# Kernel optimization log

Hardware: AMD Instinct MI355X
Metric: run time of the kernel (lower is better)

## Reference

```python
import jax, jax.numpy as jnp
import numpy as np

DISCOUNT = 0.99
HORIZON = 16


def setup_inputs() -> dict:
    key = jax.random.key(0)
    k1, k2, k3 = jax.random.split(key, 3)
    T, B = 1024, 4096
    rewards = jax.random.normal(k1, (T, B), dtype=jnp.float32)
    values = jax.random.normal(k2, (T, B), dtype=jnp.float32)
    masks = jax.random.uniform(k3, (T, B), dtype=jnp.float32)
    return {"rewards": rewards, "values": values, "masks": masks}


def _n_step_return(rewards, values, masks, gamma, horizon):
    # rewards/values/masks: [T, B]; time_axis == 0
    T = rewards.shape[0]
    rm = rewards * masks  # masked rewards
    # Pad end of time axis with zeros so every window has length `horizon`;
    # out-of-range rewards contribute 0, matching the truncated MC sum.
    pad = jnp.zeros((horizon - 1,) + rm.shape[1:], rm.dtype)
    rm_p = jnp.concatenate([rm, pad], axis=0)  # [T + horizon - 1, B]
    t = jnp.arange(T)
    idx = t[:, None] + jnp.arange(horizon)[None, :]  # [T, horizon]
    windows = rm_p[idx]  # [T, horizon, B]
    disc = jnp.asarray(gamma, rm.dtype) ** jnp.arange(horizon, dtype=rm.dtype)
    g = jnp.einsum('thb,h->tb', windows, disc)  # windowed discounted sums
    # Bootstrap: gamma^{effective_horizon} * V(s_{min(t+horizon-1, T-1)})
    eff_h = (jnp.minimum(t + horizon, T) - t).astype(rm.dtype)  # [T]
    v_idx = jnp.minimum(t + horizon - 1, T - 1)  # [T]
    g = g + (jnp.asarray(gamma, rm.dtype) ** eff_h)[:, None] * values[v_idx]
    return g


def reference(rewards, values, masks):
    return _n_step_return(rewards, values, masks, DISCOUNT, HORIZON)
```

## Files before the change

### kernel.cpp

```cpp
#include <hip/hip_runtime.h>


constexpr int   T_DIM  = 1024;
constexpr int   B_DIM  = 4096;
constexpr int   B4     = B_DIM / 4;
constexpr int   H      = 16;
constexpr int   CT     = 8;
constexpr int   HALO   = H - 1;
constexpr int   ROWS   = CT + HALO;
constexpr float GAMMA  = 0.99f;

constexpr float gpow_c(int n) {
    float g = 1.0f;
    for (int i = 0; i < n; ++i) g *= GAMMA;
    return g;
}
constexpr float G16 = gpow_c(16);

__device__ __forceinline__ float4 f4_mul(float4 a, float4 b) {
    return make_float4(a.x * b.x, a.y * b.y, a.z * b.z, a.w * b.w);
}
__device__ __forceinline__ float4 f4_fma(float s, float4 a, float4 b) {
    return make_float4(fmaf(s, a.x, b.x), fmaf(s, a.y, b.y),
                       fmaf(s, a.z, b.z), fmaf(s, a.w, b.w));
}

__global__ __launch_bounds__(256, 2)
void NStepReturn_88691074662796_kernel(const float4* __restrict__ rewards,
                                       const float4* __restrict__ values,
                                       const float4* __restrict__ masks,
                                       float4* __restrict__ out)
{
    const int b4 = blockIdx.x * 256 + threadIdx.x;
    const int t0 = blockIdx.y * CT;

    float4 rm[ROWS];
    #pragma unroll
    for (int i = 0; i < ROWS; ++i) {
        const int t = t0 + i;
        if (t < T_DIM) {
            const float4 r = rewards[t * B4 + b4];
            const float4 m = masks[t * B4 + b4];
            rm[i] = f4_mul(r, m);
        } else {
            rm[i] = make_float4(0.0f, 0.0f, 0.0f, 0.0f);
        }
    }
    float4 v[CT];
    #pragma unroll
    for (int i = 0; i < CT; ++i) {
        const int vi = min(t0 + i + H - 1, T_DIM - 1);
        v[i] = values[vi * B4 + b4];
    }

    float4 W = make_float4(0.0f, 0.0f, 0.0f, 0.0f);
    #pragma unroll
    for (int h = H - 1; h >= 0; --h) W = f4_fma(GAMMA, W, rm[CT - 1 + h]);

    {
        const int t = t0 + CT - 1;
        float gb = G16;
        if (t + H > T_DIM) {
            gb = 1.0f;
            for (int k = 0; k < T_DIM - t; ++k) gb *= GAMMA;
        }
        out[t * B4 + b4] = f4_fma(gb, v[CT - 1], W);
    }

    #pragma unroll
    for (int j = CT - 2; j >= 0; --j) {
        const int t = t0 + j;
        W = f4_fma(GAMMA, W, rm[j]);
        W = f4_fma(-G16, rm[j + H], W);

        float gb = G16;
        if (t + H > T_DIM) {
            gb = 1.0f;
            for (int k = 0; k < T_DIM - t; ++k) gb *= GAMMA;
        }
        out[t * B4 + b4] = f4_fma(gb, v[j], W);
    }
}

extern "C" void kernel_launch(void* const* d_in, const int* in_sizes, int n_in,
                              void* d_out, int out_size, void* d_ws, size_t ws_size,
                              hipStream_t stream) {
    const float4* rewards = (const float4*)d_in[0];
    const float4* values  = (const float4*)d_in[1];
    const float4* masks   = (const float4*)d_in[2];
    float4* out = (float4*)d_out;

    dim3 grid(B4 / 256, T_DIM / CT);
    dim3 block(256);
    NStepReturn_88691074662796_kernel<<<grid, block, 0, stream>>>(rewards, values, masks, out);
}
```

Baseline: 95.93 us.

## Switch to scalar per-thread columns and taller time tiles to cut halo reloads

Each thread now handles one float column instead of a float4, and each block covers 32 time steps instead of 8. All reward and mask loads are issued before the multiply. The taller tile lowers the halo overhead on rewards and masks from about 23/8 to 47/32 loads per output. In exchange, global accesses are 4-byte scalars instead of 16-byte vectors, and each thread holds many more registers (r, m, v arrays), which may hurt occupancy.

```diff
diff --git a/kernel.cpp b/kernel.cpp
--- a/kernel.cpp
+++ b/kernel.cpp
@@ -3,9 +3,8 @@
 
 constexpr int   T_DIM  = 1024;
 constexpr int   B_DIM  = 4096;
-constexpr int   B4     = B_DIM / 4;
 constexpr int   H      = 16;
-constexpr int   CT     = 8;
+constexpr int   CT     = 32;
 constexpr int   HALO   = H - 1;
 constexpr int   ROWS   = CT + HALO;
 constexpr float GAMMA  = 0.99f;
@@ -17,45 +16,39 @@
 }
 constexpr float G16 = gpow_c(16);
 
-__device__ __forceinline__ float4 f4_mul(float4 a, float4 b) {
-    return make_float4(a.x * b.x, a.y * b.y, a.z * b.z, a.w * b.w);
-}
-__device__ __forceinline__ float4 f4_fma(float s, float4 a, float4 b) {
-    return make_float4(fmaf(s, a.x, b.x), fmaf(s, a.y, b.y),
-                       fmaf(s, a.z, b.z), fmaf(s, a.w, b.w));
-}
-
 __global__ __launch_bounds__(256, 2)
-void NStepReturn_88691074662796_kernel(const float4* __restrict__ rewards,
-                                       const float4* __restrict__ values,
-                                       const float4* __restrict__ masks,
-                                       float4* __restrict__ out)
+void NStepReturn_88691074662796_kernel(const float* __restrict__ rewards,
+                                       const float* __restrict__ values,
+                                       const float* __restrict__ masks,
+                                       float* __restrict__ out)
 {
-    const int b4 = blockIdx.x * 256 + threadIdx.x;
+    const int b  = blockIdx.x * 256 + threadIdx.x;
     const int t0 = blockIdx.y * CT;
 
-    float4 rm[ROWS];
+    float r[ROWS], m[ROWS], v[CT];
     #pragma unroll
     for (int i = 0; i < ROWS; ++i) {
         const int t = t0 + i;
         if (t < T_DIM) {
-            const float4 r = rewards[t * B4 + b4];
-            const float4 m = masks[t * B4 + b4];
-            rm[i] = f4_mul(r, m);
+            r[i] = rewards[t * B_DIM + b];
+            m[i] = masks[t * B_DIM + b];
         } else {
-            rm[i] = make_float4(0.0f, 0.0f, 0.0f, 0.0f);
+            r[i] = 0.0f;
+            m[i] = 0.0f;
         }
     }
-    float4 v[CT];
     #pragma unroll
     for (int i = 0; i < CT; ++i) {
         const int vi = min(t0 + i + H - 1, T_DIM - 1);
-        v[i] = values[vi * B4 + b4];
+        v[i] = values[vi * B_DIM + b];
     }
 
-    float4 W = make_float4(0.0f, 0.0f, 0.0f, 0.0f);
     #pragma unroll
-    for (int h = H - 1; h >= 0; --h) W = f4_fma(GAMMA, W, rm[CT - 1 + h]);
+    for (int i = 0; i < ROWS; ++i) r[i] *= m[i];
+
+    float W = 0.0f;
+    #pragma unroll
+    for (int h = H - 1; h >= 0; --h) W = fmaf(GAMMA, W, r[CT - 1 + h]);
 
     {
         const int t = t0 + CT - 1;
@@ -64,33 +57,33 @@
             gb = 1.0f;
             for (int k = 0; k < T_DIM - t; ++k) gb *= GAMMA;
         }
-        out[t * B4 + b4] = f4_fma(gb, v[CT - 1], W);
+        out[t * B_DIM + b] = fmaf(gb, v[CT - 1], W);
     }
 
     #pragma unroll
     for (int j = CT - 2; j >= 0; --j) {
         const int t = t0 + j;
-        W = f4_fma(GAMMA, W, rm[j]);
-        W = f4_fma(-G16, rm[j + H], W);
+        W = fmaf(GAMMA, W, r[j]);
+        W = fmaf(-G16, r[j + H], W);
 
         float gb = G16;
         if (t + H > T_DIM) {
             gb = 1.0f;
             for (int k = 0; k < T_DIM - t; ++k) gb *= GAMMA;
         }
-        out[t * B4 + b4] = f4_fma(gb, v[j], W);
+        out[t * B_DIM + b] = fmaf(gb, v[j], W);
     }
 }
 
 extern "C" void kernel_launch(void* const* d_in, const int* in_sizes, int n_in,
                               void* d_out, int out_size, void* d_ws, size_t ws_size,
                               hipStream_t stream) {
-    const float4* rewards = (const float4*)d_in[0];
-    const float4* values  = (const float4*)d_in[1];
-    const float4* masks   = (const float4*)d_in[2];
-    float4* out = (float4*)d_out;
+    const float* rewards = (const float*)d_in[0];
+    const float* values  = (const float*)d_in[1];
+    const float* masks   = (const float*)d_in[2];
+    float* out = (float*)d_out;
 
-    dim3 grid(B4 / 256, T_DIM / CT);
+    dim3 grid(B_DIM / 256, T_DIM / CT);
     dim3 block(256);
     NStepReturn_88691074662796_kernel<<<grid, block, 0, stream>>>(rewards, values, masks, out);
 }
```

After: 89.62 us. -6.6%, faster.
